# Kernel optimization log

Measured on AMD Instinct MI355X. Metric: run time of the kernel, lower is better.

Reference implementation:

```python
import jax, jax.numpy as jnp
import numpy as np

H = 12
PD = 4
DECAY = 0.99
OFFSETS = (1, 2, 4, 8)
_PI = np.array([0, 0, 0, 1, 1, 2])  # Plucker pair indices i for G(2,4)
_PJ = np.array([1, 2, 3, 2, 3, 3])  # Plucker pair indices j
_J6 = jnp.array([[0, 0, 0, 0, 0, 1], [0, 0, 0, 0, -1, 0], [0, 0, 0, 1, 0, 0],
                 [0, 0, 1, 0, 0, 0], [0, -1, 0, 0, 0, 0], [1, 0, 0, 0, 0, 0]],
                dtype=jnp.float32)


def exterior(p1, p2):
    # p1, p2: [..., 4] -> normalized Plucker coords [..., 6]
    L = p1[..., _PI] * p2[..., _PJ] - p1[..., _PJ] * p2[..., _PI]
    n = jnp.maximum(jnp.linalg.norm(L, axis=-1, keepdims=True), 1e-12)
    return L / n


def setup_inputs() -> dict:
    key = jax.random.key(0)
    ks = jax.random.split(key, 12)
    B, T, D = 2, 2048, 768
    s = 0.02
    return {
        "x": jax.random.normal(ks[0], (B, T, D), jnp.float32),
        "qkv_w": jax.random.normal(ks[1], (3 * D, D), jnp.float32) * s,
        "qkv_b": jnp.zeros((3 * D,), jnp.float32),
        "w1_write": jax.random.normal(ks[2], (PD * H, D), jnp.float32) * s,
        "w2_write": jax.random.normal(ks[3], (PD * H, D), jnp.float32) * s,
        "w1_read": jax.random.normal(ks[4], (PD * H, D), jnp.float32) * s,
        "w2_read": jax.random.normal(ks[5], (PD * H, D), jnp.float32) * s,
        "memv_w": jax.random.normal(ks[6], (D, D), jnp.float32) * s,
        "memv_b": jnp.zeros((D,), jnp.float32),
        "memg_w": jax.random.normal(ks[7], (H, D), jnp.float32) * s,
        "memg_b": jnp.zeros((H,), jnp.float32),
        "mem_scale": jnp.full((H,), 0.1, jnp.float32),
        "out_w": jax.random.normal(ks[8], (D, D), jnp.float32) * s,
        "out_b": jnp.zeros((D,), jnp.float32),
    }


def reference(x, qkv_w, qkv_b, w1_write, w2_write, w1_read, w2_read,
              memv_w, memv_b, memg_w, memg_b, mem_scale, out_w, out_b):
    B, T, D = x.shape
    dh = D // H
    scale = dh ** -0.5

    # --- standard causal attention (dropout disabled / eval mode) ---
    qkv = (x @ qkv_w.T + qkv_b).reshape(B, T, 3, H, dh)
    qkv = jnp.transpose(qkv, (2, 0, 3, 1, 4))  # [3,B,H,T,dh]
    q, k, v = qkv[0], qkv[1], qkv[2]
    att = jnp.einsum('bhtd,bhsd->bhts', q, k) * scale
    upper = jnp.triu(jnp.ones((T, T), bool), 1)
    att = jnp.where(upper, -jnp.inf, att)
    attn = jax.nn.softmax(att, axis=-1)
    seq_out = jnp.einsum('bhts,bhsd->bhtd', attn, v)
    seq_out = jnp.transpose(seq_out, (0, 2, 1, 3)).reshape(B, T, D)

    # --- multi-scale Plucker incidence memory ---
    r1 = (x @ w1_read.T).reshape(B, T, H, PD)
    r2 = (x @ w2_read.T).reshape(B, T, H, PD)
    read_h = jnp.transpose(exterior(r1, r2), (0, 2, 1, 3))  # [B,H,T,6]

    keep = jnp.tril(jnp.ones((T, T), bool), -1)  # strict lower triangle
    total = jnp.zeros((B, H, T, T), x.dtype)
    n_active = 0
    for off in OFFSETS:
        if off >= T:
            continue
        n_active += 1
        x_past = jnp.concatenate(
            [jnp.zeros((B, off, D), x.dtype), x[:, :-off]], axis=1)
        w1 = (x_past @ w1_write.T).reshape(B, T, H, PD)
        w2 = (x @ w2_write.T).reshape(B, T, H, PD)
        wl = exterior(w1, w2)                       # [B,T,H,6]
        jw = jnp.einsum('bthi,ij->bthj', wl, _J6)   # apply J
        jw = jnp.transpose(jw, (0, 2, 1, 3))        # [B,H,T,6]
        inc = jnp.einsum('bhtp,bhsp->bhts', read_h, jw)
        total = total + jnp.where(keep, inc * inc, 0.0)
    total = total / n_active

    pos = jnp.arange(T, dtype=x.dtype)
    decay_w = jnp.where(keep, DECAY ** (pos[:, None] - pos[None, :]), 0.0)
    total = total * decay_w
    mem_score = total.sum(axis=-1)  # [B,H,T]

    mem_val = x @ memv_w.T + memv_b
    gate = jax.nn.sigmoid(x @ memg_w.T + memg_b)  # [B,T,H]
    gated = jax.nn.sigmoid(jnp.transpose(mem_score, (0, 2, 1)) * mem_scale) * gate
    gated = gated.mean(axis=-1, keepdims=True)  # [B,T,1]

    return (seq_out + gated * mem_val) @ out_w.T + out_b
```

## Files before the change

### kernel.cpp

```cpp
#include <hip/hip_runtime.h>

#define H 12
#define T 2048
#define D 768
#define NBT 4096
#define SCALE 0.125f
#define DECAY_F 0.99f
#define NCHK 72
#define NBLK_ATTN (24 * NCHK)

typedef __attribute__((ext_vector_type(8))) short bf16x8;
typedef __attribute__((ext_vector_type(4))) float f32x4;
typedef __attribute__((ext_vector_type(16))) float f32x16;

static __device__ __forceinline__ ushort f2bf(float f) {
  union { float f; unsigned u; } v; v.f = f;
  unsigned r = (v.u + 0x7FFFu + ((v.u >> 16) & 1u)) >> 16;
  return (ushort)r;
}
static __device__ __forceinline__ float bf2f(ushort u) {
  union { unsigned u; float f; } v; v.u = ((unsigned)u) << 16;
  return v.f;
}
static __device__ __forceinline__ unsigned cvtpk(float lo, float hi) {
  unsigned r;
  asm("v_cvt_pk_bf16_f32 %0, %1, %2" : "=v"(r) : "v"(lo), "v"(hi));
  return r;
}
static __device__ __forceinline__ void swap32(unsigned &a, unsigned &b) {
  asm("v_permlane32_swap_b32 %0, %1" : "+v"(a), "+v"(b));
}

static __device__ __forceinline__ void gload16(const void* g, void* s) {
  __builtin_amdgcn_global_load_lds(
      (const __attribute__((address_space(1))) unsigned int*)g,
      (__attribute__((address_space(3))) unsigned int*)s, 16, 0, 0);
}

__global__ __launch_bounds__(256) void cast_all(
    const float* __restrict__ x, const float* __restrict__ qkv_w,
    const float* __restrict__ memv_w, const float* __restrict__ out_w,
    const float* __restrict__ w1w, const float* __restrict__ w2w,
    const float* __restrict__ w1r, const float* __restrict__ w2r,
    const float* __restrict__ memg_w, ushort* __restrict__ dst)
{
  const size_t i8 = ((size_t)blockIdx.x * 256 + threadIdx.x) * 8;
  const float* src; size_t off;
  if      (i8 < 3145728) { src = x;      off = i8; }
  else if (i8 < 4915200) { src = qkv_w;  off = i8 - 3145728; }
  else if (i8 < 5505024) { src = memv_w; off = i8 - 4915200; }
  else if (i8 < 5541888) { src = w1w;    off = i8 - 5505024; }
  else if (i8 < 5578752) { src = w2w;    off = i8 - 5541888; }
  else if (i8 < 5615616) { src = w1r;    off = i8 - 5578752; }
  else if (i8 < 5652480) { src = w2r;    off = i8 - 5615616; }
  else if (i8 < 5661696) { src = memg_w; off = i8 - 5652480; }
  else if (i8 < 5701632) { *(uint4*)(dst + i8) = make_uint4(0, 0, 0, 0); return; }
  else                   { src = out_w;  off = i8 - 5701632; }
  const float4 a = *(const float4*)(src + off);
  const float4 b = *(const float4*)(src + off + 4);
  bf16x8 o;
  o[0] = (short)f2bf(a.x); o[1] = (short)f2bf(a.y);
  o[2] = (short)f2bf(a.z); o[3] = (short)f2bf(a.w);
  o[4] = (short)f2bf(b.x); o[5] = (short)f2bf(b.y);
  o[6] = (short)f2bf(b.z); o[7] = (short)f2bf(b.w);
  *(bf16x8*)(dst + i8) = o;
}

__global__ __launch_bounds__(512, 2) void gemm8_mega(
    const ushort* __restrict__ A, const ushort* __restrict__ W,
    const float* __restrict__ qkv_b, const float* __restrict__ memv_b,
    ushort* __restrict__ memvp, float* __restrict__ pw,
    float* __restrict__ pmemg,
    ushort* __restrict__ Qb, ushort* __restrict__ Kb, ushort* __restrict__ Vtb)
{
  __shared__ ushort lds[65536];
  const int tid = threadIdx.x;
  const int w = tid >> 6, l = tid & 63;
  const int wm = w >> 2, wn = w & 3;
  const int l15 = l & 15, l4 = l >> 4;

  int bid = blockIdx.x;
  bid = (bid & 7) * 26 + (bid >> 3);
  const int bx = bid % 13, by = bid / 13;
  const int bm = by * 256, bn = bx * 256;

  f32x4 acc[8][4];
#pragma unroll
  for (int i = 0; i < 8; i++)
#pragma unroll
    for (int j = 0; j < 4; j++) acc[i][j] = (f32x4){0.f, 0.f, 0.f, 0.f};

  auto stage = [&](int s, int isB, int h, int kt) {
    const ushort* src = (isB ? W + (size_t)bn * 768 : A + (size_t)bm * 768);
#pragma unroll
    for (int j = 0; j < 2; j++) {
      const int chunk = j * 512 + tid;
      const int r = chunk >> 3, c = chunk & 7;
      const int csrc = c ^ (r & 7);
      gload16(src + (size_t)(h * 128 + r) * 768 + kt * 64 + csrc * 8,
              (char*)lds + s * 65536 + isB * 32768 + h * 16384
                         + (size_t)(j * 512 + w * 64) * 16);
    }
  };
  auto rdA = [&](int s, int mi, int ks) -> bf16x8 {
    const int row = wm * 128 + mi * 16 + l15;
    const int ch = (ks * 4 + l4) ^ (l15 & 7);
    return *(const bf16x8*)((const char*)lds + s * 65536 + row * 128 + ch * 16);
  };
  auto rdB = [&](int s, int ni, int ks) -> bf16x8 {
    const int row = wn * 64 + ni * 16 + l15;
    const int ch = (ks * 4 + l4) ^ (l15 & 7);
    return *(const bf16x8*)((const char*)lds + s * 65536 + 32768 + row * 128 + ch * 16);
  };

  stage(0, 1, 0, 0); stage(0, 1, 1, 0); stage(0, 0, 0, 0); stage(0, 0, 1, 0);

#define MFMA_QUAD(mb, ks)                                                      \
  {                                                                            \
    __builtin_amdgcn_s_setprio(1);                                             \
    _Pragma("unroll")                                                          \
    for (int mi = 0; mi < 4; mi++) {                                           \
      const bf16x8 av = rdA(s, (mb) + mi, (ks));                               \
      acc[(mb)+mi][0] = __builtin_amdgcn_mfma_f32_16x16x32_bf16(av, bq0, acc[(mb)+mi][0], 0, 0, 0); \
      acc[(mb)+mi][1] = __builtin_amdgcn_mfma_f32_16x16x32_bf16(av, bq1, acc[(mb)+mi][1], 0, 0, 0); \
      acc[(mb)+mi][2] = __builtin_amdgcn_mfma_f32_16x16x32_bf16(av, bq2, acc[(mb)+mi][2], 0, 0, 0); \
      acc[(mb)+mi][3] = __builtin_amdgcn_mfma_f32_16x16x32_bf16(av, bq3, acc[(mb)+mi][3], 0, 0, 0); \
    }                                                                          \
    __builtin_amdgcn_s_setprio(0);                                             \
  }

  for (int t = 0; t < 12; t++) {
    const int s = t & 1, sn = s ^ 1;
    const int ktn = (t + 1) % 12;
    bf16x8 bq0, bq1, bq2, bq3;
    stage(sn, 1, 0, ktn);
    asm volatile("s_waitcnt vmcnt(2)" ::: "memory");
    __builtin_amdgcn_s_barrier();
    __builtin_amdgcn_sched_barrier(0);
    bq0 = rdB(s, 0, 0); bq1 = rdB(s, 1, 0); bq2 = rdB(s, 2, 0); bq3 = rdB(s, 3, 0);
    MFMA_QUAD(0, 0);
    __builtin_amdgcn_s_barrier();
    stage(sn, 1, 1, ktn);
    MFMA_QUAD(4, 0);
    __builtin_amdgcn_s_barrier();
    stage(sn, 0, 0, ktn);
    bq0 = rdB(s, 0, 1); bq1 = rdB(s, 1, 1); bq2 = rdB(s, 2, 1); bq3 = rdB(s, 3, 1);
    MFMA_QUAD(0, 1);
    __builtin_amdgcn_s_barrier();
    stage(sn, 0, 1, ktn);
    MFMA_QUAD(4, 1);
    __builtin_amdgcn_s_barrier();
  }

#pragma unroll
  for (int mi = 0; mi < 8; mi++) {
    const int row0 = bm + wm * 128 + mi * 16 + l4 * 4;
    const int b = row0 >> 11, tl = row0 & (T - 1);
#pragma unroll
    for (int ni = 0; ni < 4; ni++) {
      const int col = bn + wn * 64 + ni * 16 + l15;
      const f32x4 a4 = acc[mi][ni];
      if (col < 2304) {
        const float bv = qkv_b[col];
        const int sec = col / 768, cm = col % 768;
        const int h = cm >> 6, d = cm & 63;
        if (sec < 2) {
          ushort* dst = sec ? Kb : Qb;
#pragma unroll
          for (int r = 0; r < 4; r++)
            dst[((size_t)(b * H + h) * T + tl + r) * 64 + d] = f2bf(a4[r] + bv);
        } else {
          uint2 u;
          u.x = (unsigned)f2bf(a4[0] + bv) | ((unsigned)f2bf(a4[1] + bv) << 16);
          u.y = (unsigned)f2bf(a4[2] + bv) | ((unsigned)f2bf(a4[3] + bv) << 16);
          *(uint2*)(Vtb + ((size_t)(b * H + h) * 64 + d) * T + tl) = u;
        }
      } else if (col < 3072) {
        const int c2 = col - 2304;
        const float bv = memv_b[c2];
#pragma unroll
        for (int r = 0; r < 4; r++)
          memvp[(size_t)(row0 + r) * 768 + c2] = f2bf(a4[r] + bv);
      } else if (col < 3276) {
        const int c2 = col - 3072;
        if (c2 < 192) {
          float* pb = pw + (size_t)(c2 / 48) * (H * NBT * 4);
          const int hh = (c2 % 48) >> 2, comp = c2 & 3;
#pragma unroll
          for (int r = 0; r < 4; r++)
            pb[((size_t)hh * NBT + row0 + r) * 4 + comp] = a4[r];
        } else {
#pragma unroll
          for (int r = 0; r < 4; r++)
            pmemg[(size_t)(c2 - 192) * NBT + row0 + r] = a4[r];
        }
      }
    }
  }
}

__global__ __launch_bounds__(256) void gemm_mfma128(
    const ushort* __restrict__ A, const ushort* __restrict__ W,
    const float* __restrict__ bias, float* __restrict__ C, int ldc)
{
  __shared__ ushort A_lds[128 * 64];
  __shared__ ushort B_lds[128 * 64];
  const int tid = threadIdx.x;
  const int w = tid >> 6, l = tid & 63;
  const int wm = w >> 1, wn = w & 1;
  const int bm = blockIdx.y * 128, bn = blockIdx.x * 128;
  const int l15 = l & 15, l4 = l >> 4;

  f32x4 acc[4][4];
#pragma unroll
  for (int i = 0; i < 4; i++)
#pragma unroll
    for (int j = 0; j < 4; j++) acc[i][j] = (f32x4){0.f, 0.f, 0.f, 0.f};

  const int srow = w * 32 + (l >> 3);
  const int scol = (l & 7) * 8;
  const ushort* Ag = A + (size_t)(bm + srow) * 768 + scol;
  const ushort* Wg = W + (size_t)(bn + srow) * 768 + scol;
  ushort* Asl = &A_lds[(w * 32) * 64];
  ushort* Bsl = &B_lds[(w * 32) * 64];

  for (int k0 = 0; k0 < 768; k0 += 64) {
#pragma unroll
    for (int i = 0; i < 4; i++) {
      gload16(Ag + k0 + i * 8 * 768, Asl + i * 8 * 64);
      gload16(Wg + k0 + i * 8 * 768, Bsl + i * 8 * 64);
    }
    __syncthreads();
#pragma unroll
    for (int ks = 0; ks < 2; ks++) {
      bf16x8 af[4], bfr[4];
#pragma unroll
      for (int i = 0; i < 4; i++) {
        af[i]  = *(const bf16x8*)&A_lds[(wm * 64 + i * 16 + l15) * 64 + ks * 32 + l4 * 8];
        bfr[i] = *(const bf16x8*)&B_lds[(wn * 64 + i * 16 + l15) * 64 + ks * 32 + l4 * 8];
      }
#pragma unroll
      for (int mi = 0; mi < 4; mi++)
#pragma unroll
        for (int ni = 0; ni < 4; ni++)
          acc[mi][ni] = __builtin_amdgcn_mfma_f32_16x16x32_bf16(af[mi], bfr[ni], acc[mi][ni], 0, 0, 0);
    }
    __syncthreads();
  }
#pragma unroll
  for (int mi = 0; mi < 4; mi++) {
    const int row0 = bm + wm * 64 + mi * 16 + l4 * 4;
#pragma unroll
    for (int ni = 0; ni < 4; ni++) {
      const int col = bn + wn * 64 + ni * 16 + l15;
      const float bv = bias[col];
#pragma unroll
      for (int r = 0; r < 4; r++)
        C[(size_t)(row0 + r) * ldc + col] = acc[mi][ni][r] + bv;
    }
  }
}

__device__ __forceinline__ void ext_norm6(const float4 a, const float4 b, float* L)
{
  L[0] = a.x * b.y - a.y * b.x;
  L[1] = a.x * b.z - a.z * b.x;
  L[2] = a.x * b.w - a.w * b.x;
  L[3] = a.y * b.z - a.z * b.y;
  L[4] = a.y * b.w - a.w * b.y;
  L[5] = a.z * b.w - a.w * b.z;
  float n2 = L[0]*L[0] + L[1]*L[1] + L[2]*L[2] + L[3]*L[3] + L[4]*L[4] + L[5]*L[5];
  float n = fmaxf(sqrtf(n2), 1e-12f);
  float inv = 1.f / n;
#pragma unroll
  for (int i = 0; i < 6; i++) L[i] *= inv;
}

static __device__ void memscan_body(
    int bb, char* smem,
    const float* __restrict__ pw, const float* __restrict__ pmemg,
    const float* __restrict__ memg_b, const float* __restrict__ mem_scale,
    float* __restrict__ gate12)
{
  const int b = bb / H, h = bb % H;
  const int tid = threadIdx.x;
  float (*S)[22] = (float(*)[22])smem;
  const int base = tid * 8;
  const size_t hb = (size_t)h * NBT + (size_t)b * T;
  const float* pw1w = pw + 0 * (size_t)(H * NBT * 4) + hb * 4;
  const float* pw2w = pw + 1 * (size_t)(H * NBT * 4) + hb * 4;
  const float* pw1r = pw + 2 * (size_t)(H * NBT * 4) + hb * 4;
  const float* pw2r = pw + 3 * (size_t)(H * NBT * 4) + hb * 4;

  float M[21];
#pragma unroll
  for (int c = 0; c < 21; c++) M[c] = 0.f;
  float sloc[8];

  for (int j = 0; j < 8; j++) {
    const int t = base + j;
    const float4 w2 = *(const float4*)(pw2w + (size_t)t * 4);
    float C[21];
#pragma unroll
    for (int c = 0; c < 21; c++) C[c] = 0.f;
    const int offs[4] = {1, 2, 4, 8};
#pragma unroll
    for (int oi = 0; oi < 4; oi++) {
      const int off = offs[oi];
      if (t >= off) {
        const float4 w1 = *(const float4*)(pw1w + (size_t)(t - off) * 4);
        float L[6];
        ext_norm6(w1, w2, L);
        const float Jv[6] = { L[5], -L[4], L[3], L[2], -L[1], L[0] };
        int c = 0;
#pragma unroll
        for (int p = 0; p < 6; p++)
#pragma unroll
          for (int q = p; q < 6; q++) { C[c] += Jv[p] * Jv[q]; c++; }
      }
    }
    float R[6];
    {
      const float4 r1 = *(const float4*)(pw1r + (size_t)t * 4);
      const float4 r2 = *(const float4*)(pw2r + (size_t)t * 4);
      ext_norm6(r1, r2, R);
    }
    float qd = 0.f;
    {
      int c = 0;
#pragma unroll
      for (int p = 0; p < 6; p++) {
        qd += M[c] * R[p] * R[p]; c++;
#pragma unroll
        for (int q = p + 1; q < 6; q++) { qd += 2.f * M[c] * R[p] * R[q]; c++; }
      }
    }
    sloc[j] = qd;
#pragma unroll
    for (int cc = 0; cc < 21; cc++) M[cc] = DECAY_F * (M[cc] + C[cc]);
  }

#pragma unroll
  for (int c = 0; c < 21; c++) S[tid][c] = M[c];
  __syncthreads();
  float p8 = 0.92274469442792013f;
  for (int off = 1; off < 256; off <<= 1) {
    float tmpv[21];
#pragma unroll
    for (int c = 0; c < 21; c++) tmpv[c] = (tid >= off) ? S[tid - off][c] : 0.f;
    __syncthreads();
#pragma unroll
    for (int c = 0; c < 21; c++) S[tid][c] += p8 * tmpv[c];
    __syncthreads();
    p8 *= p8;
  }
  float P[21];
#pragma unroll
  for (int c = 0; c < 21; c++) P[c] = (tid > 0) ? S[tid - 1][c] : 0.f;

  const float msc = mem_scale[h];
  const float gb = memg_b[h];
  const size_t rb = (size_t)b * T;
  float dj = 1.f;
  for (int j = 0; j < 8; j++) {
    const int t = base + j;
    float R[6];
    {
      const float4 r1 = *(const float4*)(pw1r + (size_t)t * 4);
      const float4 r2 = *(const float4*)(pw2r + (size_t)t * 4);
      ext_norm6(r1, r2, R);
    }
    float qd = 0.f;
    {
      int c = 0;
#pragma unroll
      for (int p = 0; p < 6; p++) {
        qd += P[c] * R[p] * R[p]; c++;
#pragma unroll
        for (int q = p + 1; q < 6; q++) { qd += 2.f * P[c] * R[p] * R[q]; c++; }
      }
    }
    const float score = (sloc[j] + dj * qd) * 0.25f;
    const float g1 = 1.f / (1.f + __expf(-score * msc));
    const float graw = pmemg[hb + t] + gb;
    const float g2 = 1.f / (1.f + __expf(-graw));
    gate12[(rb + t) * H + h] = g1 * g2;
    dj *= DECAY_F;
  }
}

__global__ __launch_bounds__(256) void attn_memscan(
    const ushort* __restrict__ Qb, const ushort* __restrict__ Kb,
    const ushort* __restrict__ Vtb, ushort* __restrict__ o_part,
    float* __restrict__ rs_part,
    const float* __restrict__ pw, const float* __restrict__ pmemg,
    const float* __restrict__ memg_b, const float* __restrict__ mem_scale,
    float* __restrict__ gate12)
{
  __shared__ __align__(16) char smem[36864];

  if (blockIdx.x < 24) {
    memscan_body(blockIdx.x, smem, pw, pmemg, memg_b, mem_scale, gate12);
    return;
  }
  const int abid = blockIdx.x - 24;

  typedef ushort row72[72];
  row72* K_lds = (row72*)smem;
  row72* V_lds = (row72*)(smem + 18432);

  const int bh = abid / NCHK;
  const int ci2 = 71 - (abid % NCHK);
  int ci = ci2;
  int qb = 15;
#pragma unroll
  for (int q = 0; q < 16; q++) {
    const int cnt = (q >> 1) + 1;
    if (ci < cnt) { qb = q; break; }
    ci -= cnt;
  }
  const int slot = bh * NCHK + ci2;
  const int t0 = qb * 128;
  const int it0 = ci * 4;
  const int it1 = min(it0 + 4, 2 * qb + 2);

  const int tid = threadIdx.x;
  const int w = tid >> 6;
  const int l = tid & 63;
  const int l31 = l & 31;
  const int lhi = l >> 5;

  bf16x8 qf[4];
  {
    const ushort* qp = Qb + ((size_t)bh * T + t0 + w * 32 + l31) * 64 + 8 * lhi;
#pragma unroll
    for (int kf = 0; kf < 4; kf++) qf[kf] = *(const bf16x8*)(qp + kf * 16);
  }
  f32x16 o0, o1;
#pragma unroll
  for (int r = 0; r < 16; r++) { o0[r] = 0.f; o1[r] = 0.f; }
  float rs = 0.f;

  const int sr = tid >> 2;
  const int scg = (tid & 3) * 16;
  const ushort* ksrc = Kb + ((size_t)bh * T + sr) * 64 + scg;
  const ushort* vsrc = Vtb + ((size_t)bh * 64 + sr) * T + scg;
  const int qlo = t0 + w * 32;
  const int qg = qlo + l31;

  bf16x8 kA0, kA1, vA0, vA1, kB0, kB1, vB0, vB1;
  {
    const size_t sa = (size_t)it0 * 64, sb = sa + 64;
    kA0 = *(const bf16x8*)(ksrc + sa * 64);
    kA1 = *(const bf16x8*)(ksrc + sa * 64 + 8);
    vA0 = *(const bf16x8*)(vsrc + sa);
    vA1 = *(const bf16x8*)(vsrc + sa + 8);
    kB0 = *(const bf16x8*)(ksrc + sb * 64);
    kB1 = *(const bf16x8*)(ksrc + sb * 64 + 8);
    vB0 = *(const bf16x8*)(vsrc + sb);
    vB1 = *(const bf16x8*)(vsrc + sb + 8);
  }

  auto process = [&](int s0, int ro) {
    f32x16 sA, sB;
#pragma unroll
    for (int r = 0; r < 16; r++) { sA[r] = 0.f; sB[r] = 0.f; }
    __builtin_amdgcn_s_setprio(1);
#pragma unroll
    for (int kf = 0; kf < 4; kf++) {
      const bf16x8 ka  = *(const bf16x8*)&K_lds[ro + l31][kf * 16 + 8 * lhi];
      const bf16x8 kb2 = *(const bf16x8*)&K_lds[ro + 32 + l31][kf * 16 + 8 * lhi];
      sA = __builtin_amdgcn_mfma_f32_32x32x16_bf16(ka, qf[kf], sA, 0, 0, 0);
      sB = __builtin_amdgcn_mfma_f32_32x32x16_bf16(kb2, qf[kf], sB, 0, 0, 0);
    }
    __builtin_amdgcn_s_setprio(0);

    const bool nomask = (s0 + 63 <= qlo);
#pragma unroll
    for (int half = 0; half < 2; half++) {
      float pv[16];
#pragma unroll
      for (int r = 0; r < 16; r++) {
        const int srow = (r & 3) + 8 * (r >> 2) + 4 * lhi;
        const float sv = (half == 0) ? sA[r] : sB[r];
        float p = __expf(sv * SCALE);
        if (!nomask && (s0 + half * 32 + srow > qg)) p = 0.f;
        rs += p;
        pv[r] = p;
      }
#pragma unroll
      for (int sub = 0; sub < 2; sub++) {
        const float* p8 = pv + 8 * sub;
        unsigned X = cvtpk(p8[0], p8[1]);
        unsigned Y = cvtpk(p8[4], p8[5]);
        unsigned Z = cvtpk(p8[2], p8[3]);
        unsigned Wd = cvtpk(p8[6], p8[7]);
        swap32(X, Y);
        swap32(Z, Wd);
        union { unsigned u[4]; bf16x8 v; } fr;
        fr.u[0] = X; fr.u[1] = Z; fr.u[2] = Y; fr.u[3] = Wd;
        const int ksl = half * 2 + sub;
        const bf16x8 va = *(const bf16x8*)&V_lds[ro + l31][ksl * 16 + 8 * lhi];
        const bf16x8 vb = *(const bf16x8*)&V_lds[ro + 32 + l31][ksl * 16 + 8 * lhi];
        __builtin_amdgcn_s_setprio(1);
        o0 = __builtin_amdgcn_mfma_f32_32x32x16_bf16(va, fr.v, o0, 0, 0, 0);
        o1 = __builtin_amdgcn_mfma_f32_32x32x16_bf16(vb, fr.v, o1, 0, 0, 0);
        __builtin_amdgcn_s_setprio(0);
      }
    }
  };

  for (int its = it0; its < it1; its += 2) {
    __syncthreads();
    *(bf16x8*)&K_lds[sr][scg]       = kA0;
    *(bf16x8*)&K_lds[sr][scg + 8]   = kA1;
    *(bf16x8*)&V_lds[sr][scg]       = vA0;
    *(bf16x8*)&V_lds[sr][scg + 8]   = vA1;
    *(bf16x8*)&K_lds[64 + sr][scg]     = kB0;
    *(bf16x8*)&K_lds[64 + sr][scg + 8] = kB1;
    *(bf16x8*)&V_lds[64 + sr][scg]     = vB0;
    *(bf16x8*)&V_lds[64 + sr][scg + 8] = vB1;
    __syncthreads();
    if (its + 2 < it1) {
      const size_t sa = (size_t)(its + 2) * 64, sb = sa + 64;
      kA0 = *(const bf16x8*)(ksrc + sa * 64);
      kA1 = *(const bf16x8*)(ksrc + sa * 64 + 8);
      vA0 = *(const bf16x8*)(vsrc + sa);
      vA1 = *(const bf16x8*)(vsrc + sa + 8);
      kB0 = *(const bf16x8*)(ksrc + sb * 64);
      kB1 = *(const bf16x8*)(ksrc + sb * 64 + 8);
      vB0 = *(const bf16x8*)(vsrc + sb);
      vB1 = *(const bf16x8*)(vsrc + sb + 8);
    }
    const int s0A = its * 64, s0B = s0A + 64;
    if (s0A <= qlo + 31) process(s0A, 0);
    if (s0B <= qlo + 31) process(s0B, 64);
  }

  rs += __shfl_xor(rs, 32);

  const int brow = w * 32 + l31;
  ushort* ob = o_part + ((size_t)slot * 128 + brow) * 64;
  float* rsb = rs_part + (size_t)slot * 128;
#pragma unroll
  for (int r = 0; r < 16; r += 2) {
    const int d = (r & 3) + 8 * (r >> 2) + 4 * lhi;
    *(unsigned*)(ob + d)      = cvtpk(o0[r], o0[r + 1]);
    *(unsigned*)(ob + 32 + d) = cvtpk(o1[r], o1[r + 1]);
  }
  if (l < 32) rsb[brow] = rs;
}

__global__ __launch_bounds__(256) void reduce_fuse(
    const ushort* __restrict__ o_part, const float* __restrict__ rs_part,
    const ushort* __restrict__ memv, const float* __restrict__ gate12,
    ushort* __restrict__ zb)
{
  const int idx = blockIdx.x * 256 + threadIdx.x;
  const int row = idx / 96, c = (idx % 96) * 8;
  const int h = c >> 6, d0 = c & 63;
  const int b = row >> 11, tl = row & (T - 1);
  const int qb = tl >> 7, rloc = tl & 127;
  const int m = qb >> 1;
  const int cnt = m + 1;
  const int base = m * (m + 1) + (qb & 1) * (m + 1);
  const size_t bid0 = (size_t)(b * H + h) * NCHK + base;

  float o[8] = {0.f, 0.f, 0.f, 0.f, 0.f, 0.f, 0.f, 0.f};
  float rsum = 0.f;
  for (int ci = 0; ci < cnt; ci++) {
    const bf16x8 pv = *(const bf16x8*)(o_part + ((bid0 + ci) * 128 + rloc) * 64 + d0);
#pragma unroll
    for (int j = 0; j < 8; j++) o[j] += bf2f((ushort)pv[j]);
    rsum += rs_part[(bid0 + ci) * 128 + rloc];
  }
  const float inv = 1.f / rsum;

  const float* gp = gate12 + (size_t)row * H;
  float gs = 0.f;
#pragma unroll
  for (int j = 0; j < 12; j++) gs += gp[j];
  const float g = gs * (1.f / 12.f);

  const bf16x8 mv = *(const bf16x8*)(memv + (size_t)row * D + c);
  bf16x8 z;
#pragma unroll
  for (int j = 0; j < 8; j++)
    z[j] = (short)f2bf(o[j] * inv + g * bf2f((ushort)mv[j]));
  *(bf16x8*)(zb + (size_t)row * D + c) = z;
}

extern "C" void kernel_launch(void* const* d_in, const int* in_sizes, int n_in,
                              void* d_out, int out_size, void* d_ws, size_t ws_size,
                              hipStream_t stream)
{
  const float* x      = (const float*)d_in[0];
  const float* qkv_w  = (const float*)d_in[1];
  const float* qkv_b  = (const float*)d_in[2];
  const float* w1w    = (const float*)d_in[3];
  const float* w2w    = (const float*)d_in[4];
  const float* w1r    = (const float*)d_in[5];
  const float* w2r    = (const float*)d_in[6];
  const float* memv_w = (const float*)d_in[7];
  const float* memv_b = (const float*)d_in[8];
  const float* memg_w = (const float*)d_in[9];
  const float* memg_b = (const float*)d_in[10];
  const float* mem_scale = (const float*)d_in[11];
  const float* out_w  = (const float*)d_in[12];
  const float* out_b  = (const float*)d_in[13];
  float* out = (float*)d_out;

  float* ws    = (float*)d_ws;
  float* pw    = ws;
  float* pmemg = pw + (size_t)4 * H * NBT * 4;
  float* gate12 = pmemg + (size_t)H * NBT;
  float* rs_part = gate12 + (size_t)NBT * H;
  ushort* memv = (ushort*)(rs_part + (size_t)NBLK_ATTN * 128);
  ushort* Xb  = memv + (size_t)NBT * D;
  ushort* Wb  = Xb + (size_t)NBT * D;
  ushort* Qb  = Wb + (size_t)NBT * D;
  ushort* Kb  = Qb + (size_t)24 * T * 64;
  ushort* Vtb = Kb + (size_t)24 * T * 64;
  ushort* zb  = Vtb + (size_t)24 * T * 64;
  ushort* o_part = zb + (size_t)NBT * D;

  const ushort* W_out = Wb + (size_t)3328 * 768;

  dim3 blk(256);
  cast_all<<<dim3(3072), blk, 0, stream>>>(x, qkv_w, memv_w, out_w,
                                           w1w, w2w, w1r, w2r, memg_w, Xb);

  gemm8_mega<<<dim3(16 * 13), dim3(512), 0, stream>>>(
      Xb, Wb, qkv_b, memv_b, memv, pw, pmemg, Qb, Kb, Vtb);

  attn_memscan<<<dim3(NBLK_ATTN + 24), blk, 0, stream>>>(
      Qb, Kb, Vtb, o_part, rs_part, pw, pmemg, memg_b, mem_scale, gate12);

  reduce_fuse<<<dim3(NBT * 96 / 256), blk, 0, stream>>>(o_part, rs_part, memv,
                                                        gate12, zb);
  gemm_mfma128<<<dim3(6, 32), blk, 0, stream>>>(zb, W_out, out_b, out, 768);
}
```

Before: 113.5 us.

## Split memory scan across more blocks and narrow output GEMM tiles

The memory-score decayed scan, previously done by 24 blocks each walking 2048 steps serially, is split into 192 blocks, one per 256-step chunk. Each block writes per-token partial scores and a chunk carry, and a new small gatescan kernel combines the carries and computes the gates. The output GEMM tile shrinks from 128x128 to 128x64, doubling the grid to 384 blocks so more CUs are busy. The cost is an extra kernel launch plus extra workspace traffic for the partials, and the narrower tiles reuse each loaded A tile less.

```diff
diff --git a/kernel.cpp b/kernel.cpp
--- a/kernel.cpp
+++ b/kernel.cpp
@@ -8,6 +8,7 @@
 #define DECAY_F 0.99f
 #define NCHK 72
 #define NBLK_ATTN (24 * NCHK)
+#define NBLK_MS1 192
 
 typedef __attribute__((ext_vector_type(8))) short bf16x8;
 typedef __attribute__((ext_vector_type(4))) float f32x4;
@@ -199,50 +200,53 @@
   }
 }
 
-__global__ __launch_bounds__(256) void gemm_mfma128(
+__global__ __launch_bounds__(256) void gemm_out64(
     const ushort* __restrict__ A, const ushort* __restrict__ W,
-    const float* __restrict__ bias, float* __restrict__ C, int ldc)
+    const float* __restrict__ bias, float* __restrict__ C)
 {
   __shared__ ushort A_lds[128 * 64];
-  __shared__ ushort B_lds[128 * 64];
+  __shared__ ushort B_lds[64 * 64];
   const int tid = threadIdx.x;
   const int w = tid >> 6, l = tid & 63;
   const int wm = w >> 1, wn = w & 1;
-  const int bm = blockIdx.y * 128, bn = blockIdx.x * 128;
+  const int bm = blockIdx.y * 128, bn = blockIdx.x * 64;
   const int l15 = l & 15, l4 = l >> 4;
 
-  f32x4 acc[4][4];
+  f32x4 acc[4][2];
 #pragma unroll
   for (int i = 0; i < 4; i++)
 #pragma unroll
-    for (int j = 0; j < 4; j++) acc[i][j] = (f32x4){0.f, 0.f, 0.f, 0.f};
-
-  const int srow = w * 32 + (l >> 3);
+    for (int j = 0; j < 2; j++) acc[i][j] = (f32x4){0.f, 0.f, 0.f, 0.f};
+
+  const int srowA = w * 32 + (l >> 3);
+  const int srowB = w * 16 + (l >> 3);
   const int scol = (l & 7) * 8;
-  const ushort* Ag = A + (size_t)(bm + srow) * 768 + scol;
-  const ushort* Wg = W + (size_t)(bn + srow) * 768 + scol;
+  const ushort* Ag = A + (size_t)(bm + srowA) * 768 + scol;
+  const ushort* Wg = W + (size_t)(bn + srowB) * 768 + scol;
   ushort* Asl = &A_lds[(w * 32) * 64];
-  ushort* Bsl = &B_lds[(w * 32) * 64];
+  ushort* Bsl = &B_lds[(w * 16) * 64];
 
   for (int k0 = 0; k0 < 768; k0 += 64) {
 #pragma unroll
-    for (int i = 0; i < 4; i++) {
+    for (int i = 0; i < 4; i++)
       gload16(Ag + k0 + i * 8 * 768, Asl + i * 8 * 64);
+#pragma unroll
+    for (int i = 0; i < 2; i++)
       gload16(Wg + k0 + i * 8 * 768, Bsl + i * 8 * 64);
-    }
     __syncthreads();
 #pragma unroll
     for (int ks = 0; ks < 2; ks++) {
-      bf16x8 af[4], bfr[4];
-#pragma unroll
-      for (int i = 0; i < 4; i++) {
-        af[i]  = *(const bf16x8*)&A_lds[(wm * 64 + i * 16 + l15) * 64 + ks * 32 + l4 * 8];
-        bfr[i] = *(const bf16x8*)&B_lds[(wn * 64 + i * 16 + l15) * 64 + ks * 32 + l4 * 8];
-      }
+      bf16x8 af[4], bfr[2];
+#pragma unroll
+      for (int i = 0; i < 4; i++)
+        af[i] = *(const bf16x8*)&A_lds[(wm * 64 + i * 16 + l15) * 64 + ks * 32 + l4 * 8];
+#pragma unroll
+      for (int i = 0; i < 2; i++)
+        bfr[i] = *(const bf16x8*)&B_lds[(wn * 32 + i * 16 + l15) * 64 + ks * 32 + l4 * 8];
 #pragma unroll
       for (int mi = 0; mi < 4; mi++)
 #pragma unroll
-        for (int ni = 0; ni < 4; ni++)
+        for (int ni = 0; ni < 2; ni++)
           acc[mi][ni] = __builtin_amdgcn_mfma_f32_16x16x32_bf16(af[mi], bfr[ni], acc[mi][ni], 0, 0, 0);
     }
     __syncthreads();
@@ -251,12 +255,12 @@
   for (int mi = 0; mi < 4; mi++) {
     const int row0 = bm + wm * 64 + mi * 16 + l4 * 4;
 #pragma unroll
-    for (int ni = 0; ni < 4; ni++) {
-      const int col = bn + wn * 64 + ni * 16 + l15;
+    for (int ni = 0; ni < 2; ni++) {
+      const int col = bn + wn * 32 + ni * 16 + l15;
       const float bv = bias[col];
 #pragma unroll
       for (int r = 0; r < 4; r++)
-        C[(size_t)(row0 + r) * ldc + col] = acc[mi][ni][r] + bv;
+        C[(size_t)(row0 + r) * 768 + col] = acc[mi][ni][r] + bv;
     }
   }
 }
@@ -276,33 +280,26 @@
   for (int i = 0; i < 6; i++) L[i] *= inv;
 }
 
-static __device__ void memscan_body(
-    int bb, char* smem,
-    const float* __restrict__ pw, const float* __restrict__ pmemg,
-    const float* __restrict__ memg_b, const float* __restrict__ mem_scale,
-    float* __restrict__ gate12)
-{
-  const int b = bb / H, h = bb % H;
+static __device__ void memscan1_body(
+    int bb, char* smem, const float* __restrict__ pw,
+    float* __restrict__ Rp, float* __restrict__ G)
+{
+  const int bh = bb >> 3, chunk = bb & 7;
+  const int b = bh / H, h = bh % H;
   const int tid = threadIdx.x;
   float (*S)[22] = (float(*)[22])smem;
-  const int base = tid * 8;
+  const int t = chunk * 256 + tid;
   const size_t hb = (size_t)h * NBT + (size_t)b * T;
   const float* pw1w = pw + 0 * (size_t)(H * NBT * 4) + hb * 4;
   const float* pw2w = pw + 1 * (size_t)(H * NBT * 4) + hb * 4;
   const float* pw1r = pw + 2 * (size_t)(H * NBT * 4) + hb * 4;
   const float* pw2r = pw + 3 * (size_t)(H * NBT * 4) + hb * 4;
 
-  float M[21];
-#pragma unroll
-  for (int c = 0; c < 21; c++) M[c] = 0.f;
-  float sloc[8];
-
-  for (int j = 0; j < 8; j++) {
-    const int t = base + j;
+  float Cm[21];
+#pragma unroll
+  for (int c = 0; c < 21; c++) Cm[c] = 0.f;
+  {
     const float4 w2 = *(const float4*)(pw2w + (size_t)t * 4);
-    float C[21];
-#pragma unroll
-    for (int c = 0; c < 21; c++) C[c] = 0.f;
     const int offs[4] = {1, 2, 4, 8};
 #pragma unroll
     for (int oi = 0; oi < 4; oi++) {
@@ -316,94 +313,65 @@
 #pragma unroll
         for (int p = 0; p < 6; p++)
 #pragma unroll
-          for (int q = p; q < 6; q++) { C[c] += Jv[p] * Jv[q]; c++; }
+          for (int q = p; q < 6; q++) { Cm[c] += Jv[p] * Jv[q]; c++; }
       }
     }
-    float R[6];
-    {
-      const float4 r1 = *(const float4*)(pw1r + (size_t)t * 4);
-      const float4 r2 = *(const float4*)(pw2r + (size_t)t * 4);
-      ext_norm6(r1, r2, R);
-    }
-    float qd = 0.f;
-    {
-      int c = 0;
-#pragma unroll
-      for (int p = 0; p < 6; p++) {
-        qd += M[c] * R[p] * R[p]; c++;
-#pragma unroll
-        for (int q = p + 1; q < 6; q++) { qd += 2.f * M[c] * R[p] * R[q]; c++; }
-      }
-    }
-    sloc[j] = qd;
-#pragma unroll
-    for (int cc = 0; cc < 21; cc++) M[cc] = DECAY_F * (M[cc] + C[cc]);
-  }
-
-#pragma unroll
-  for (int c = 0; c < 21; c++) S[tid][c] = M[c];
+  }
+  float R[6];
+  {
+    const float4 r1 = *(const float4*)(pw1r + (size_t)t * 4);
+    const float4 r2 = *(const float4*)(pw2r + (size_t)t * 4);
+    ext_norm6(r1, r2, R);
+  }
+
+#pragma unroll
+  for (int c = 0; c < 21; c++) S[tid][c] = Cm[c];
   __syncthreads();
-  float p8 = 0.92274469442792013f;
+  float pd = DECAY_F;
   for (int off = 1; off < 256; off <<= 1) {
     float tmpv[21];
 #pragma unroll
     for (int c = 0; c < 21; c++) tmpv[c] = (tid >= off) ? S[tid - off][c] : 0.f;
     __syncthreads();
 #pragma unroll
-    for (int c = 0; c < 21; c++) S[tid][c] += p8 * tmpv[c];
+    for (int c = 0; c < 21; c++) S[tid][c] += pd * tmpv[c];
     __syncthreads();
-    p8 *= p8;
+    pd *= pd;
   }
   float P[21];
 #pragma unroll
-  for (int c = 0; c < 21; c++) P[c] = (tid > 0) ? S[tid - 1][c] : 0.f;
-
-  const float msc = mem_scale[h];
-  const float gb = memg_b[h];
-  const size_t rb = (size_t)b * T;
-  float dj = 1.f;
-  for (int j = 0; j < 8; j++) {
-    const int t = base + j;
-    float R[6];
-    {
-      const float4 r1 = *(const float4*)(pw1r + (size_t)t * 4);
-      const float4 r2 = *(const float4*)(pw2r + (size_t)t * 4);
-      ext_norm6(r1, r2, R);
-    }
-    float qd = 0.f;
-    {
-      int c = 0;
-#pragma unroll
-      for (int p = 0; p < 6; p++) {
-        qd += P[c] * R[p] * R[p]; c++;
-#pragma unroll
-        for (int q = p + 1; q < 6; q++) { qd += 2.f * P[c] * R[p] * R[q]; c++; }
-      }
-    }
-    const float score = (sloc[j] + dj * qd) * 0.25f;
-    const float g1 = 1.f / (1.f + __expf(-score * msc));
-    const float graw = pmemg[hb + t] + gb;
-    const float g2 = 1.f / (1.f + __expf(-graw));
-    gate12[(rb + t) * H + h] = g1 * g2;
-    dj *= DECAY_F;
-  }
+  for (int c = 0; c < 21; c++) P[c] = (tid > 0) ? DECAY_F * S[tid - 1][c] : 0.f;
+
+  float part1 = 0.f;
+  {
+    int c = 0;
+#pragma unroll
+    for (int p = 0; p < 6; p++) {
+      part1 += P[c] * R[p] * R[p]; c++;
+#pragma unroll
+      for (int q = p + 1; q < 6; q++) { part1 += 2.f * P[c] * R[p] * R[q]; c++; }
+    }
+  }
+  float* rp = Rp + ((size_t)bh * T + t) * 8;
+  *(float4*)rp = make_float4(R[0], R[1], R[2], R[3]);
+  *(float4*)(rp + 4) = make_float4(R[4], R[5], part1, 0.f);
+  if (tid < 21)
+    G[((size_t)bh * 8 + chunk) * 21 + tid] = S[255][tid];
 }
 
 __global__ __launch_bounds__(256) void attn_memscan(
     const ushort* __restrict__ Qb, const ushort* __restrict__ Kb,
     const ushort* __restrict__ Vtb, ushort* __restrict__ o_part,
     float* __restrict__ rs_part,
-    const float* __restrict__ pw, const float* __restrict__ pmemg,
-    const float* __restrict__ memg_b, const float* __restrict__ mem_scale,
-    float* __restrict__ gate12)
+    const float* __restrict__ pw, float* __restrict__ Rp, float* __restrict__ G)
 {
   __shared__ __align__(16) char smem[36864];
 
-  if (blockIdx.x < 24) {
-    memscan_body(blockIdx.x, smem, pw, pmemg, memg_b, mem_scale, gate12);
+  if (blockIdx.x < NBLK_MS1) {
+    memscan1_body(blockIdx.x, smem, pw, Rp, G);
     return;
   }
-  const int abid = blockIdx.x - 24;
+  const int abid = blockIdx.x - NBLK_MS1;
 
   typedef ushort row72[72];
   row72* K_lds = (row72*)smem;
@@ -551,6 +519,61 @@
   if (l < 32) rsb[brow] = rs;
 }
 
+__global__ __launch_bounds__(256) void gatescan(
+    const float* __restrict__ G, const float* __restrict__ Rp,
+    const float* __restrict__ pmemg, const float* __restrict__ memg_b,
+    const float* __restrict__ mem_scale, float* __restrict__ gate12)
+{
+  __shared__ float E[8][21];
+  const int bh = blockIdx.x;
+  const int b = bh / H, h = bh % H;
+  const int tid = threadIdx.x;
+  if (tid < 21) {
+    float e = 0.f;
+    const float d256 = 0.076314145f;
+    for (int c = 0; c < 8; c++) {
+      E[c][tid] = e;
+      e = DECAY_F * G[((size_t)bh * 8 + c) * 21 + tid] + d256 * e;
+    }
+  }
+  __syncthreads();
+  const int chunk = tid >> 5;
+  const int base = (tid & 31) * 8;
+  float Ec[21];
+#pragma unroll
+  for (int c = 0; c < 21; c++) Ec[c] = E[chunk][c];
+
+  const float msc = mem_scale[h];
+  const float gb = memg_b[h];
+  const size_t hb = (size_t)h * NBT + (size_t)b * T;
+  const size_t rb = (size_t)b * T;
+  float dj = __powf(DECAY_F, (float)base);
+  for (int j = 0; j < 8; j++) {
+    const int tl = chunk * 256 + base + j;
+    const float* rp = Rp + ((size_t)bh * T + tl) * 8;
+    const float4 q0 = *(const float4*)rp;
+    const float4 q1 = *(const float4*)(rp + 4);
+    const float R[6] = { q0.x, q0.y, q0.z, q0.w, q1.x, q1.y };
+    const float part1 = q1.z;
+    float qd = 0.f;
+    {
+      int c = 0;
+#pragma unroll
+      for (int p = 0; p < 6; p++) {
+        qd += Ec[c] * R[p] * R[p]; c++;
+#pragma unroll
+        for (int q = p + 1; q < 6; q++) { qd += 2.f * Ec[c] * R[p] * R[q]; c++; }
+      }
+    }
+    const float score = (part1 + dj * qd) * 0.25f;
+    const float g1 = 1.f / (1.f + __expf(-score * msc));
+    const float graw = pmemg[hb + tl] + gb;
+    const float g2 = 1.f / (1.f + __expf(-graw));
+    gate12[(rb + tl) * H + h] = g1 * g2;
+    dj *= DECAY_F;
+  }
+}
+
 __global__ __launch_bounds__(256) void reduce_fuse(
     const ushort* __restrict__ o_part, const float* __restrict__ rs_part,
     const ushort* __restrict__ memv, const float* __restrict__ gate12,
@@ -615,7 +638,9 @@
   float* pmemg = pw + (size_t)4 * H * NBT * 4;
   float* gate12 = pmemg + (size_t)H * NBT;
   float* rs_part = gate12 + (size_t)NBT * H;
-  ushort* memv = (ushort*)(rs_part + (size_t)NBLK_ATTN * 128);
+  float* Rp    = rs_part + (size_t)NBLK_ATTN * 128;
+  float* G     = Rp + (size_t)24 * T * 8;
+  ushort* memv = (ushort*)(G + 24 * 8 * 21 + 24);
   ushort* Xb  = memv + (size_t)NBT * D;
   ushort* Wb  = Xb + (size_t)NBT * D;
   ushort* Qb  = Wb + (size_t)NBT * D;
@@ -633,10 +658,12 @@
   gemm8_mega<<<dim3(16 * 13), dim3(512), 0, stream>>>(
       Xb, Wb, qkv_b, memv_b, memv, pw, pmemg, Qb, Kb, Vtb);
 
-  attn_memscan<<<dim3(NBLK_ATTN + 24), blk, 0, stream>>>(
-      Qb, Kb, Vtb, o_part, rs_part, pw, pmemg, memg_b, mem_scale, gate12);
+  attn_memscan<<<dim3(NBLK_ATTN + NBLK_MS1), blk, 0, stream>>>(
+      Qb, Kb, Vtb, o_part, rs_part, pw, Rp, G);
+
+  gatescan<<<dim3(24), blk, 0, stream>>>(G, Rp, pmemg, memg_b, mem_scale, gate12);
 
   reduce_fuse<<<dim3(NBT * 96 / 256), blk, 0, stream>>>(o_part, rs_part, memv,
                                                         gate12, zb);
-  gemm_mfma128<<<dim3(6, 32), blk, 0, stream>>>(zb, W_out, out_b, out, 768);
-}
+  gemm_out64<<<dim3(12, 32), blk, 0, stream>>>(zb, W_out, out_b, out);
+}
```

After: 123.3 us. 8.6% more time.
